# Kernel optimization log

Measured on AMD Instinct MI355X. Metric: run time of the kernel, lower is better.

Reference implementation:

```python
import jax, jax.numpy as jnp
import numpy as np
from jax import lax

B, L, D, H, NW, NL = 4, 256, 768, 384, 4, 9
WINDOWS = (3, 5, 7, 9)


def setup_inputs() -> dict:
    key = jax.random.key(0)
    ks = jax.random.split(key, 12)
    s = 0.05
    return {
        "seq_out": jax.random.normal(ks[0], (B, L, D), jnp.float32),
        "valid_ids": jax.random.randint(ks[1], (B, L), 0, 2),
        "w_ih_f": jax.random.normal(ks[2], (NW, 4 * H, D), jnp.float32) * s,
        "w_hh_f": jax.random.normal(ks[3], (NW, 4 * H, H), jnp.float32) * s,
        "b_ih_f": jax.random.normal(ks[4], (NW, 4 * H), jnp.float32) * s,
        "b_hh_f": jax.random.normal(ks[5], (NW, 4 * H), jnp.float32) * s,
        "w_ih_b": jax.random.normal(ks[6], (NW, 4 * H, D), jnp.float32) * s,
        "w_hh_b": jax.random.normal(ks[7], (NW, 4 * H, H), jnp.float32) * s,
        "b_ih_b": jax.random.normal(ks[8], (NW, 4 * H), jnp.float32) * s,
        "b_hh_b": jax.random.normal(ks[9], (NW, 4 * H), jnp.float32) * s,
        "lin_w": jax.random.normal(ks[10], (NL, D), jnp.float32) * s,
        "lin_b": jnp.zeros((NL,), jnp.float32),
    }


def _lstm_last(win, mask, W_ih, W_hh, b, reverse):
    # invalid (out-of-range) steps leave the state untouched, so the final
    # carry equals the hidden state after the last valid step (PyTorch LSTM math).
    Bx, Lx, w, Dx = win.shape
    Hh = W_hh.shape[1]

    def step(carry, xm):
        h, c = carry
        x_t, m = xm  # [B,L,D], [L]
        gates = x_t @ W_ih.T + h @ W_hh.T + b  # [B,L,4H], gate order i,f,g,o
        i, f, g, o = jnp.split(gates, 4, axis=-1)
        i = jax.nn.sigmoid(i)
        f = jax.nn.sigmoid(f)
        g = jnp.tanh(g)
        o = jax.nn.sigmoid(o)
        c_new = f * c + i * g
        h_new = o * jnp.tanh(c_new)
        m3 = m[None, :, None]
        return (jnp.where(m3, h_new, h), jnp.where(m3, c_new, c)), None

    init = (jnp.zeros((Bx, Lx, Hh), win.dtype), jnp.zeros((Bx, Lx, Hh), win.dtype))
    (h, _), _ = lax.scan(step, init, (jnp.moveaxis(win, 2, 0), mask.T), reverse=reverse)
    return h


def _window_features(x, w, Wif, Whf, bf, Wib, Whb, bb):
    # Faithful vectorization of windows_sequence: the sorted index_list for
    # position i is the contiguous slice [max(0,i-w//2) .. min(L-1,i+w//2)].
    Bx, Lx, Dx = x.shape
    half = w // 2
    pos = jnp.arange(Lx)[:, None] + jnp.arange(-half, half + 1)[None, :]  # [L,w]
    mask = (pos >= 0) & (pos < Lx)
    idx = jnp.clip(pos, 0, Lx - 1)
    win = x[:, idx, :]  # [B,L,w,D]
    h_f = _lstm_last(win, mask, Wif, Whf, bf, reverse=False)  # fwd dir: last output
    h_b = _lstm_last(win, mask, Wib, Whb, bb, reverse=True)   # bwd dir over reversed window
    return jnp.concatenate([h_f, h_b], axis=-1)  # [B,L,D]


def _valid_scatter(x, valid_ids):
    # Left-pack tokens with valid_ids==1 (the nested Python scatter loop).
    Bx, Lx, Dx = x.shape
    v = valid_ids.astype(jnp.int32)
    dest = jnp.where(v == 1, jnp.cumsum(v, axis=1) - 1, Lx)  # invalid -> pad slot

    def pack(row_x, row_d):
        return jnp.zeros((Lx + 1, Dx), row_x.dtype).at[row_d].set(row_x)[:Lx]

    return jax.vmap(pack)(x, dest)


def reference(seq_out, valid_ids, w_ih_f, w_hh_f, b_ih_f, b_hh_f,
              w_ih_b, w_hh_b, b_ih_b, b_hh_b, lin_w, lin_b):
    x = _valid_scatter(seq_out, valid_ids)  # [B,L,D]; dropout is identity in eval
    locals_ = [
        _window_features(x, WINDOWS[i],
                         w_ih_f[i], w_hh_f[i], b_ih_f[i] + b_hh_f[i],
                         w_ih_b[i], w_hh_b[i], b_ih_b[i] + b_hh_b[i])
        for i in range(NW)
    ]
    muti = jnp.stack(locals_, axis=2)  # [B,L,NW,D]
    # dot-att: query is the (packed) sequence output itself
    attn = jax.nn.softmax(
        jnp.einsum('bld,blwd->blw', x, muti) / jnp.sqrt(jnp.float32(D)), axis=-1)
    local_feat = jnp.einsum('blw,blwd->bld', attn, muti)
    out = x + local_feat
    return out @ lin_w.T + lin_b  # logits [B,L,NL]
```

## Files before the change

### kernel.cpp

```cpp
#include <hip/hip_runtime.h>
#include <math.h>

#define LL 256
#define DD 768
#define HH 384
#define G4 1536
#define NWIN 4
#define NLIN 9
#define NPOS 1024
#define PROJ_N 12288
#define HSTRIDE 520

typedef __attribute__((ext_vector_type(8))) short short8;
typedef __attribute__((ext_vector_type(4))) short short4v;
typedef __attribute__((ext_vector_type(16))) float f32x16;

static __device__ __forceinline__ float bf2f(unsigned short u) {
    union { unsigned int i; float f; } v; v.i = ((unsigned int)u) << 16; return v.f;
}
static __device__ __forceinline__ unsigned short f2bf(float f) {
    unsigned int u = __float_as_uint(f);
    u += 0x7fff + ((u >> 16) & 1);
    return (unsigned short)(u >> 16);
}
static __device__ __forceinline__ float fsig(float x) {
    return __builtin_amdgcn_rcpf(1.f + __expf(-x));
}
static __device__ __forceinline__ float ftanh(float x) {
    return 1.f - 2.f * __builtin_amdgcn_rcpf(1.f + __expf(2.f * x));
}

__global__ __launch_bounds__(256) void prep_kernel(
        const float* __restrict__ seq, const int* __restrict__ valid,
        unsigned short* __restrict__ xfrag,
        const float* __restrict__ wihF, const float* __restrict__ wihB,
        unsigned short* __restrict__ wfih,
        const float* __restrict__ whhF, const float* __restrict__ whhB,
        unsigned short* __restrict__ wfhh) {
    const int tid = threadIdx.x;
    if (blockIdx.x < 128) {
        const int b = blockIdx.x >> 5;
        const int chunk = blockIdx.x & 31;
        __shared__ int vbuf[LL];
        __shared__ int dest[LL];
        __shared__ int nvalid;
        vbuf[tid] = valid[b * LL + tid];
        __syncthreads();
        if (tid == 0) {
            int c = 0;
            for (int l = 0; l < LL; ++l) dest[l] = vbuf[l] ? c++ : -1;
            nvalid = c;
        }
        __syncthreads();
        const int nv = nvalid;
        for (int l = chunk * 8; l < chunk * 8 + 8; ++l) {
            const int d = dest[l];
            if (d >= 0) {
                const float* src = seq + (size_t)(b * LL + l) * DD;
                const int pos = b * LL + d;
                const int pt = pos >> 5, pl = pos & 31;
                for (int j = tid; j < DD / 8; j += 256) {
                    const float4 v0 = ((const float4*)src)[2 * j];
                    const float4 v1 = ((const float4*)src)[2 * j + 1];
                    short8 pv;
                    pv[0] = (short)f2bf(v0.x); pv[1] = (short)f2bf(v0.y);
                    pv[2] = (short)f2bf(v0.z); pv[3] = (short)f2bf(v0.w);
                    pv[4] = (short)f2bf(v1.x); pv[5] = (short)f2bf(v1.y);
                    pv[6] = (short)f2bf(v1.z); pv[7] = (short)f2bf(v1.w);
                    *(short8*)(xfrag + ((size_t)(pt * 48 + (j >> 1)) * 512 + (pl + 32 * (j & 1)) * 8)) = pv;
                }
            }
            if (l >= nv) {
                const int pos = b * LL + l;
                const int pt = pos >> 5, pl = pos & 31;
                const short8 zv = {};
                for (int j = tid; j < DD / 8; j += 256)
                    *(short8*)(xfrag + ((size_t)(pt * 48 + (j >> 1)) * 512 + (pl + 32 * (j & 1)) * 8)) = zv;
            }
        }
    } else {
        __shared__ unsigned short lds[32 * 768];
        const int cb = blockIdx.x - 128;
        const int isIH = cb < 384;
        const int vblk = isIH ? cb : (cb - 384);
        const int K = isIH ? DD : HH;
        const float* srcF = isIH ? wihF : whhF;
        const float* srcB = isIH ? wihB : whhB;
        unsigned short* dst = isIH ? wfih : wfhh;
        const int vrow0 = vblk * 32;
        const int chain = vrow0 / G4;
        const int dir = chain >> 2, wi = chain & 3;
        const float* src = (dir ? srcB : srcF) + (size_t)(wi * G4 + (vrow0 % G4)) * K;
        const int total = 32 * K;
        for (int i = tid * 4; i < total; i += 1024) {
            const float4 v = *(const float4*)(src + i);
            lds[i + 0] = f2bf(v.x); lds[i + 1] = f2bf(v.y);
            lds[i + 2] = f2bf(v.z); lds[i + 3] = f2bf(v.w);
        }
        __syncthreads();
        const int nks = K >> 4;
        for (int slot = tid; slot < nks * 64; slot += 256) {
            const int ks = slot >> 6;
            const int lane = slot & 63;
            const int row = lane & 31;
            const int kb = ks * 16 + (lane >> 5) * 8;
            const short8 v = *(const short8*)&lds[row * K + kb];
            *(short8*)(dst + ((size_t)vblk * nks + ks) * 512 + lane * 8) = v;
        }
    }
}

__global__ __launch_bounds__(256) void proj_mfma(
        const unsigned short* __restrict__ xf,
        const unsigned short* __restrict__ wf,
        const float* __restrict__ bihf, const float* __restrict__ bhhf,
        const float* __restrict__ bihb, const float* __restrict__ bhhb,
        unsigned short* __restrict__ proj) {
    __shared__ __align__(16) unsigned short st[4 * 4096];
    const int wv = threadIdx.x >> 6;
    const int lane = threadIdx.x & 63;
    const int colid = lane & 31, hq = lane >> 5;
    const int chain = blockIdx.x & 7;
    const int r8 = blockIdx.x >> 3;
    const int us = r8 % 12;
    const int mtg = r8 / 12;
    const int dir = chain >> 2, wi = chain & 3;

    const unsigned short* bP = wf + (size_t)((chain * 48 + wv * 12 + us) * 48) * 512 + lane * 8;
    const unsigned short* aP = xf + (size_t)(mtg * 4 * 48) * 512 + lane * 8;

    f32x16 acc[4] = {};
#pragma unroll 4
    for (int ks = 0; ks < 48; ++ks) {
        const short8 bv = *(const short8*)(bP + ks * 512);
        const short8 a0 = *(const short8*)(aP + (0 * 48 + ks) * 512);
        const short8 a1 = *(const short8*)(aP + (1 * 48 + ks) * 512);
        const short8 a2 = *(const short8*)(aP + (2 * 48 + ks) * 512);
        const short8 a3 = *(const short8*)(aP + (3 * 48 + ks) * 512);
        acc[0] = __builtin_amdgcn_mfma_f32_32x32x16_bf16(a0, bv, acc[0], 0, 0, 0);
        acc[1] = __builtin_amdgcn_mfma_f32_32x32x16_bf16(a1, bv, acc[1], 0, 0, 0);
        acc[2] = __builtin_amdgcn_mfma_f32_32x32x16_bf16(a2, bv, acc[2], 0, 0, 0);
        acc[3] = __builtin_amdgcn_mfma_f32_32x32x16_bf16(a3, bv, acc[3], 0, 0, 0);
    }
    const int br = wv * HH + us * 32 + colid;
    const float bv = (dir ? bihb : bihf)[wi * G4 + br] + (dir ? bhhb : bhhf)[wi * G4 + br];
#pragma unroll
    for (int i = 0; i < 4; ++i) {
#pragma unroll
        for (int r = 0; r < 16; ++r) {
            const int row = (r & 3) + 8 * (r >> 2) + 4 * hq;
            st[i * 4096 + (row * 32 + colid) * 4 + wv] = f2bf(acc[i][r] + bv);
        }
    }
    __syncthreads();
#pragma unroll
    for (int j = 0; j < 8; ++j) {
        const int idx = j * 256 + threadIdx.x;
        const int i = idx >> 9, rem = idx & 511;
        const int pl = rem >> 4, q = rem & 15;
        const int pos = (mtg * 4 + i) * 32 + pl;
        *(int4*)(proj + (size_t)pos * PROJ_N + chain * G4 + us * 128 + q * 8) =
            ((const int4*)st)[idx];
    }
}

__global__ __launch_bounds__(768, 3) void lstm_fused(
        const unsigned short* __restrict__ Wf,
        const unsigned short* __restrict__ proj,
        unsigned short* __restrict__ hfin) {
    const int p = blockIdx.x & 3, sub = (blockIdx.x >> 2) & 1;
    const int slot = blockIdx.x >> 3;
    const int chainA[4] = {3, 7, 2, 6};
    const int chainB[4] = {0, 4, 1, 5};
    const int chain = (slot < 16) ? chainA[p] : chainB[p];
    const int pt = sub * 16 + (slot & 15);
    const int dir = chain >> 2, wi = chain & 3;
    const int w = 3 + 2 * wi, half = wi + 1;
    const int tid = threadIdx.x;
    const int lane = tid & 63, wv = tid >> 6;
    const int colid = lane & 31, hq = lane >> 5;
    const int uu = wv * 32 + colid;
    const int m0 = pt * 32, b = m0 >> 8, l0 = m0 & 255;

    __shared__ __align__(16) unsigned short Hbuf[2][24 * HSTRIDE];
    float c[16];
#pragma unroll
    for (int r = 0; r < 16; ++r) c[r] = 0.f;

    const unsigned short* projb = proj + (size_t)(b * LL) * PROJ_N + chain * G4 + uu * 4;
    const unsigned short* Wb = Wf + (size_t)((chain * 48 + wv) * 24) * 512 + lane * 8;
    const int ksp = uu >> 4, khp = (uu >> 3) & 1, jp = uu & 7;
    const int hslot = ksp * HSTRIDE + khp * 256 + jp;

    for (int s = 0; s < w; ++s) {
        const int t = dir ? (w - 1 - s) : s;
        const int tmh = t - half;
        unsigned short* cur = Hbuf[s & 1];
        const unsigned short* prev = Hbuf[(s & 1) ^ 1];

        short4v pj[16];
#pragma unroll
        for (int r = 0; r < 16; ++r) {
            const int row = (r & 3) + 8 * (r >> 2) + 4 * hq;
            int src = l0 + row + tmh;
            src = src < 0 ? 0 : (src > LL - 1 ? LL - 1 : src);
            pj[r] = __builtin_nontemporal_load((const short4v*)(projb + src * PROJ_N));
        }

        f32x16 acc0 = {}, acc1 = {}, acc2 = {}, acc3 = {};
        if (s > 0) {
            const unsigned short* Alds = prev + lane * 8;
#pragma unroll 4
            for (int ks = 0; ks < 24; ++ks) {
                const short8 av  = *(const short8*)(Alds + ks * HSTRIDE);
                const short8 bv0 = *(const short8*)(Wb + (size_t)(0 * 288 + ks) * 512);
                const short8 bv1 = *(const short8*)(Wb + (size_t)(1 * 288 + ks) * 512);
                const short8 bv2 = *(const short8*)(Wb + (size_t)(2 * 288 + ks) * 512);
                const short8 bv3 = *(const short8*)(Wb + (size_t)(3 * 288 + ks) * 512);
                acc0 = __builtin_amdgcn_mfma_f32_32x32x16_bf16(av, bv0, acc0, 0, 0, 0);
                acc1 = __builtin_amdgcn_mfma_f32_32x32x16_bf16(av, bv1, acc1, 0, 0, 0);
                acc2 = __builtin_amdgcn_mfma_f32_32x32x16_bf16(av, bv2, acc2, 0, 0, 0);
                acc3 = __builtin_amdgcn_mfma_f32_32x32x16_bf16(av, bv3, acc3, 0, 0, 0);
            }
        }

#pragma unroll
        for (int r = 0; r < 16; ++r) {
            const int row = (r & 3) + 8 * (r >> 2) + 4 * hq;
            const int src = l0 + row + tmh;
            unsigned short hv;
            if (src >= 0 && src < LL) {
                const float gi = acc0[r] + bf2f((unsigned short)pj[r][0]);
                const float gf = acc1[r] + bf2f((unsigned short)pj[r][1]);
                const float gg = acc2[r] + bf2f((unsigned short)pj[r][2]);
                const float go = acc3[r] + bf2f((unsigned short)pj[r][3]);
                c[r] = fsig(gf) * c[r] + fsig(gi) * ftanh(gg);
                hv = f2bf(fsig(go) * ftanh(c[r]));
            } else {
                hv = (s == 0) ? (unsigned short)0 : prev[hslot + row * 8];
            }
            cur[hslot + row * 8] = hv;
        }
        __syncthreads();
    }

    const unsigned short* fin = Hbuf[(w - 1) & 1];
    unsigned short* ho = hfin + (size_t)chain * (NPOS * HH) + (size_t)pt * 12288;
#pragma unroll
    for (int i = tid; i < 1536; i += 768) {
        const int ks = i >> 6, off = i & 63;
        *(int4*)(ho + ks * 512 + off * 8) = *(const int4*)(fin + ks * HSTRIDE + off * 8);
    }
}

__global__ __launch_bounds__(512) void attn_out_kernel(
        const unsigned short* __restrict__ xfrag,
        const unsigned short* __restrict__ hfin,
        const float* __restrict__ lin_w, const float* __restrict__ lin_b,
        float* __restrict__ out) {
    const int pt = blockIdx.x;
    const int tid = threadIdx.x;
    const int lane = tid & 63, wv = tid >> 6;
    const int dir = wv >> 2, kr = wv & 3;
    const int pos = lane & 31, kh = lane >> 5;
    const float inv_sqrt_d = 0.03608439182435161f;

    __shared__ float scp[8][4][32];
    __shared__ float attw[4][32];
    __shared__ float redp[8][32][10];

    const unsigned short* xb = xfrag + ((size_t)(pt * 48 + 24 * dir)) * 512 + lane * 8;
    const unsigned short* hb0 = hfin + (size_t)(dir * 4) * (NPOS * HH) + (size_t)pt * 12288 + lane * 8;

    float sc4[4] = {0.f, 0.f, 0.f, 0.f};
#pragma unroll
    for (int k = 0; k < 6; ++k) {
        const int ks = kr * 6 + k;
        const short8 xv = *(const short8*)(xb + ks * 512);
        float xf[8];
#pragma unroll
        for (int j = 0; j < 8; ++j) xf[j] = bf2f((unsigned short)xv[j]);
#pragma unroll
        for (int wi = 0; wi < 4; ++wi) {
            const short8 hv = *(const short8*)(hb0 + (size_t)wi * (NPOS * HH) + ks * 512);
#pragma unroll
            for (int j = 0; j < 8; ++j)
                sc4[wi] = fmaf(xf[j], bf2f((unsigned short)hv[j]), sc4[wi]);
        }
    }
#pragma unroll
    for (int wi = 0; wi < 4; ++wi) sc4[wi] += __shfl_down(sc4[wi], 32);
    if (lane < 32) {
#pragma unroll
        for (int wi = 0; wi < 4; ++wi) scp[wv][wi][pos] = sc4[wi];
    }
    __syncthreads();
    if (tid < 32) {
        float s[4], mx = -1e30f;
#pragma unroll
        for (int wi = 0; wi < 4; ++wi) {
            float v = 0.f;
#pragma unroll
            for (int g = 0; g < 8; ++g) v += scp[g][wi][tid];
            s[wi] = v * inv_sqrt_d;
            mx = fmaxf(mx, s[wi]);
        }
        float denom = 0.f;
#pragma unroll
        for (int wi = 0; wi < 4; ++wi) { s[wi] = __expf(s[wi] - mx); denom += s[wi]; }
        const float rd = __builtin_amdgcn_rcpf(denom);
#pragma unroll
        for (int wi = 0; wi < 4; ++wi) attw[wi][tid] = s[wi] * rd;
    }
    __syncthreads();

    float aw[4];
#pragma unroll
    for (int wi = 0; wi < 4; ++wi) aw[wi] = attw[wi][pos];
    float rp[9];
#pragma unroll
    for (int r = 0; r < 9; ++r) rp[r] = 0.f;
#pragma unroll
    for (int k = 0; k < 6; ++k) {
        const int ks = kr * 6 + k;
        const short8 xv = *(const short8*)(xb + ks * 512);
        float ov[8];
#pragma unroll
        for (int j = 0; j < 8; ++j) ov[j] = bf2f((unsigned short)xv[j]);
#pragma unroll
        for (int wi = 0; wi < 4; ++wi) {
            const short8 hv = *(const short8*)(hb0 + (size_t)wi * (NPOS * HH) + ks * 512);
#pragma unroll
            for (int j = 0; j < 8; ++j)
                ov[j] = fmaf(aw[wi], bf2f((unsigned short)hv[j]), ov[j]);
        }
        const int dbase = dir * 384 + ks * 16 + kh * 8;
#pragma unroll
        for (int r = 0; r < 9; ++r) {
            const float4 lw0 = *(const float4*)(lin_w + r * DD + dbase);
            const float4 lw1 = *(const float4*)(lin_w + r * DD + dbase + 4);
            rp[r] += ov[0] * lw0.x + ov[1] * lw0.y + ov[2] * lw0.z + ov[3] * lw0.w
                   + ov[4] * lw1.x + ov[5] * lw1.y + ov[6] * lw1.z + ov[7] * lw1.w;
        }
    }
#pragma unroll
    for (int r = 0; r < 9; ++r) rp[r] += __shfl_down(rp[r], 32);
    if (lane < 32) {
#pragma unroll
        for (int r = 0; r < 9; ++r) redp[wv][pos][r] = rp[r];
    }
    __syncthreads();
    if (tid < 288) {
        const int p2 = tid / 9, r = tid % 9;
        float s = lin_b[r];
#pragma unroll
        for (int g = 0; g < 8; ++g) s += redp[g][p2][r];
        out[(size_t)(pt * 32 + p2) * NLIN + r] = s;
    }
}

extern "C" void kernel_launch(void* const* d_in, const int* in_sizes, int n_in,
                              void* d_out, int out_size, void* d_ws, size_t ws_size,
                              hipStream_t stream) {
    (void)in_sizes; (void)n_in; (void)out_size; (void)ws_size;
    const float* seq   = (const float*)d_in[0];
    const int*   valid = (const int*)d_in[1];
    const float* wih_f = (const float*)d_in[2];
    const float* whh_f = (const float*)d_in[3];
    const float* bih_f = (const float*)d_in[4];
    const float* bhh_f = (const float*)d_in[5];
    const float* wih_b = (const float*)d_in[6];
    const float* whh_b = (const float*)d_in[7];
    const float* bih_b = (const float*)d_in[8];
    const float* bhh_b = (const float*)d_in[9];
    const float* lin_w = (const float*)d_in[10];
    const float* lin_b = (const float*)d_in[11];
    float* out = (float*)d_out;

    unsigned short* xfrag = (unsigned short*)d_ws;
    unsigned short* proj  = xfrag + (size_t)NPOS * DD;
    unsigned short* wfhh  = proj + (size_t)NPOS * PROJ_N;
    unsigned short* wfih  = wfhh + (size_t)4718592;
    unsigned short* hfin  = wfih + (size_t)9437184;

    prep_kernel<<<896, 256, 0, stream>>>(seq, valid, xfrag,
                                         wih_f, wih_b, wfih,
                                         whh_f, whh_b, wfhh);
    proj_mfma<<<768, 256, 0, stream>>>(xfrag, wfih, bih_f, bhh_f, bih_b, bhh_b, proj);
    lstm_fused<<<256, 768, 0, stream>>>(wfhh, proj, hfin);
    attn_out_kernel<<<32, 512, 0, stream>>>(xfrag, hfin, lin_w, lin_b, out);
}
```

Before: 290.0 us.

## Process two 32-row M tiles per LSTM block, splitting gate MFMAs into two passes

```diff
diff --git a/kernel.cpp b/kernel.cpp
--- a/kernel.cpp
+++ b/kernel.cpp
@@ -168,24 +168,23 @@
         const unsigned short* __restrict__ Wf,
         const unsigned short* __restrict__ proj,
         unsigned short* __restrict__ hfin) {
-    const int p = blockIdx.x & 3, sub = (blockIdx.x >> 2) & 1;
-    const int slot = blockIdx.x >> 3;
-    const int chainA[4] = {3, 7, 2, 6};
-    const int chainB[4] = {0, 4, 1, 5};
-    const int chain = (slot < 16) ? chainA[p] : chainB[p];
-    const int pt = sub * 16 + (slot & 15);
+    const int x = blockIdx.x & 7;
+    const int s0 = blockIdx.x >> 3;
+    const int pr = x >> 1;
+    int lc = (pr & 1) ? 7 : 3; if (pr & 2) lc -= 1;
+    int sc = ((pr & 1) ? 4 : 0) + ((pr & 2) ? 1 : 0);
+    const int chain = (s0 < 8) ? lc : sc;
+    const int pt64 = (x & 1) * 8 + (s0 & 7);
     const int dir = chain >> 2, wi = chain & 3;
     const int w = 3 + 2 * wi, half = wi + 1;
     const int tid = threadIdx.x;
     const int lane = tid & 63, wv = tid >> 6;
     const int colid = lane & 31, hq = lane >> 5;
     const int uu = wv * 32 + colid;
-    const int m0 = pt * 32, b = m0 >> 8, l0 = m0 & 255;
-
-    __shared__ __align__(16) unsigned short Hbuf[2][24 * HSTRIDE];
-    float c[16];
-#pragma unroll
-    for (int r = 0; r < 16; ++r) c[r] = 0.f;
+    const int m0 = pt64 * 64, b = m0 >> 8, l0 = m0 & 255;
+
+    __shared__ __align__(16) unsigned short Hbuf[2][2 * 24 * HSTRIDE];
+    f32x16 c0 = {}, c1 = {};
 
     const unsigned short* projb = proj + (size_t)(b * LL) * PROJ_N + chain * G4 + uu * 4;
     const unsigned short* Wb = Wf + (size_t)((chain * 48 + wv) * 24) * 512 + lane * 8;
@@ -198,58 +197,140 @@
         unsigned short* cur = Hbuf[s & 1];
         const unsigned short* prev = Hbuf[(s & 1) ^ 1];
 
-        short4v pj[16];
-#pragma unroll
-        for (int r = 0; r < 16; ++r) {
-            const int row = (r & 3) + 8 * (r >> 2) + 4 * hq;
-            int src = l0 + row + tmh;
-            src = src < 0 ? 0 : (src > LL - 1 ? LL - 1 : src);
-            pj[r] = __builtin_nontemporal_load((const short4v*)(projb + src * PROJ_N));
-        }
-
-        f32x16 acc0 = {}, acc1 = {}, acc2 = {}, acc3 = {};
+        f32x16 ai0 = {}, ai1 = {}, af0 = {}, af1 = {};
         if (s > 0) {
-            const unsigned short* Alds = prev + lane * 8;
+            const unsigned short* A0 = prev + lane * 8;
+            const unsigned short* A1 = prev + 24 * HSTRIDE + lane * 8;
 #pragma unroll 4
             for (int ks = 0; ks < 24; ++ks) {
-                const short8 av  = *(const short8*)(Alds + ks * HSTRIDE);
-                const short8 bv0 = *(const short8*)(Wb + (size_t)(0 * 288 + ks) * 512);
-                const short8 bv1 = *(const short8*)(Wb + (size_t)(1 * 288 + ks) * 512);
-                const short8 bv2 = *(const short8*)(Wb + (size_t)(2 * 288 + ks) * 512);
-                const short8 bv3 = *(const short8*)(Wb + (size_t)(3 * 288 + ks) * 512);
-                acc0 = __builtin_amdgcn_mfma_f32_32x32x16_bf16(av, bv0, acc0, 0, 0, 0);
-                acc1 = __builtin_amdgcn_mfma_f32_32x32x16_bf16(av, bv1, acc1, 0, 0, 0);
-                acc2 = __builtin_amdgcn_mfma_f32_32x32x16_bf16(av, bv2, acc2, 0, 0, 0);
-                acc3 = __builtin_amdgcn_mfma_f32_32x32x16_bf16(av, bv3, acc3, 0, 0, 0);
-            }
-        }
-
-#pragma unroll
-        for (int r = 0; r < 16; ++r) {
-            const int row = (r & 3) + 8 * (r >> 2) + 4 * hq;
-            const int src = l0 + row + tmh;
-            unsigned short hv;
-            if (src >= 0 && src < LL) {
-                const float gi = acc0[r] + bf2f((unsigned short)pj[r][0]);
-                const float gf = acc1[r] + bf2f((unsigned short)pj[r][1]);
-                const float gg = acc2[r] + bf2f((unsigned short)pj[r][2]);
-                const float go = acc3[r] + bf2f((unsigned short)pj[r][3]);
-                c[r] = fsig(gf) * c[r] + fsig(gi) * ftanh(gg);
-                hv = f2bf(fsig(go) * ftanh(c[r]));
-            } else {
-                hv = (s == 0) ? (unsigned short)0 : prev[hslot + row * 8];
-            }
-            cur[hslot + row * 8] = hv;
+                const short8 av0 = *(const short8*)(A0 + ks * HSTRIDE);
+                const short8 av1 = *(const short8*)(A1 + ks * HSTRIDE);
+                const short8 bvi = *(const short8*)(Wb + (size_t)(0 * 288 + ks) * 512);
+                const short8 bvf = *(const short8*)(Wb + (size_t)(1 * 288 + ks) * 512);
+                ai0 = __builtin_amdgcn_mfma_f32_32x32x16_bf16(av0, bvi, ai0, 0, 0, 0);
+                ai1 = __builtin_amdgcn_mfma_f32_32x32x16_bf16(av1, bvi, ai1, 0, 0, 0);
+                af0 = __builtin_amdgcn_mfma_f32_32x32x16_bf16(av0, bvf, af0, 0, 0, 0);
+                af1 = __builtin_amdgcn_mfma_f32_32x32x16_bf16(av1, bvf, af1, 0, 0, 0);
+            }
+        }
+        f32x16 si0, si1;
+        {
+            unsigned int pj[16];
+#pragma unroll
+            for (int r = 0; r < 16; ++r) {
+                const int row = (r & 3) + 8 * (r >> 2) + 4 * hq;
+                int src = l0 + row + tmh;
+                src = src < 0 ? 0 : (src > LL - 1 ? LL - 1 : src);
+                pj[r] = __builtin_nontemporal_load((const unsigned int*)(projb + src * PROJ_N));
+            }
+#pragma unroll
+            for (int r = 0; r < 16; ++r) {
+                const int row = (r & 3) + 8 * (r >> 2) + 4 * hq;
+                const int src = l0 + row + tmh;
+                if (src >= 0 && src < LL) {
+                    si0[r] = fsig(ai0[r] + bf2f((unsigned short)(pj[r] & 0xffff)));
+                    c0[r] = c0[r] * fsig(af0[r] + bf2f((unsigned short)(pj[r] >> 16)));
+                }
+            }
+        }
+        {
+            unsigned int pj[16];
+#pragma unroll
+            for (int r = 0; r < 16; ++r) {
+                const int row = (r & 3) + 8 * (r >> 2) + 4 * hq;
+                int src = l0 + 32 + row + tmh;
+                src = src < 0 ? 0 : (src > LL - 1 ? LL - 1 : src);
+                pj[r] = __builtin_nontemporal_load((const unsigned int*)(projb + src * PROJ_N));
+            }
+#pragma unroll
+            for (int r = 0; r < 16; ++r) {
+                const int row = (r & 3) + 8 * (r >> 2) + 4 * hq;
+                const int src = l0 + 32 + row + tmh;
+                if (src >= 0 && src < LL) {
+                    si1[r] = fsig(ai1[r] + bf2f((unsigned short)(pj[r] & 0xffff)));
+                    c1[r] = c1[r] * fsig(af1[r] + bf2f((unsigned short)(pj[r] >> 16)));
+                }
+            }
+        }
+
+        f32x16 ag0 = {}, ag1 = {}, ao0 = {}, ao1 = {};
+        if (s > 0) {
+            const unsigned short* A0 = prev + lane * 8;
+            const unsigned short* A1 = prev + 24 * HSTRIDE + lane * 8;
+#pragma unroll 4
+            for (int ks = 0; ks < 24; ++ks) {
+                const short8 av0 = *(const short8*)(A0 + ks * HSTRIDE);
+                const short8 av1 = *(const short8*)(A1 + ks * HSTRIDE);
+                const short8 bvg = *(const short8*)(Wb + (size_t)(2 * 288 + ks) * 512);
+                const short8 bvo = *(const short8*)(Wb + (size_t)(3 * 288 + ks) * 512);
+                ag0 = __builtin_amdgcn_mfma_f32_32x32x16_bf16(av0, bvg, ag0, 0, 0, 0);
+                ag1 = __builtin_amdgcn_mfma_f32_32x32x16_bf16(av1, bvg, ag1, 0, 0, 0);
+                ao0 = __builtin_amdgcn_mfma_f32_32x32x16_bf16(av0, bvo, ao0, 0, 0, 0);
+                ao1 = __builtin_amdgcn_mfma_f32_32x32x16_bf16(av1, bvo, ao1, 0, 0, 0);
+            }
+        }
+        {
+            unsigned int pj[16];
+#pragma unroll
+            for (int r = 0; r < 16; ++r) {
+                const int row = (r & 3) + 8 * (r >> 2) + 4 * hq;
+                int src = l0 + row + tmh;
+                src = src < 0 ? 0 : (src > LL - 1 ? LL - 1 : src);
+                pj[r] = __builtin_nontemporal_load((const unsigned int*)(projb + src * PROJ_N + 2));
+            }
+#pragma unroll
+            for (int r = 0; r < 16; ++r) {
+                const int row = (r & 3) + 8 * (r >> 2) + 4 * hq;
+                const int src = l0 + row + tmh;
+                unsigned short hv;
+                if (src >= 0 && src < LL) {
+                    const float tg = ftanh(ag0[r] + bf2f((unsigned short)(pj[r] & 0xffff)));
+                    const float so = fsig(ao0[r] + bf2f((unsigned short)(pj[r] >> 16)));
+                    c0[r] = fmaf(si0[r], tg, c0[r]);
+                    hv = f2bf(so * ftanh(c0[r]));
+                } else {
+                    hv = (s == 0) ? (unsigned short)0 : prev[hslot + row * 8];
+                }
+                cur[hslot + row * 8] = hv;
+            }
+        }
+        {
+            unsigned int pj[16];
+#pragma unroll
+            for (int r = 0; r < 16; ++r) {
+                const int row = (r & 3) + 8 * (r >> 2) + 4 * hq;
+                int src = l0 + 32 + row + tmh;
+                src = src < 0 ? 0 : (src > LL - 1 ? LL - 1 : src);
+                pj[r] = __builtin_nontemporal_load((const unsigned int*)(projb + src * PROJ_N + 2));
+            }
+#pragma unroll
+            for (int r = 0; r < 16; ++r) {
+                const int row = (r & 3) + 8 * (r >> 2) + 4 * hq;
+                const int src = l0 + 32 + row + tmh;
+                unsigned short hv;
+                if (src >= 0 && src < LL) {
+                    const float tg = ftanh(ag1[r] + bf2f((unsigned short)(pj[r] & 0xffff)));
+                    const float so = fsig(ao1[r] + bf2f((unsigned short)(pj[r] >> 16)));
+                    c1[r] = fmaf(si1[r], tg, c1[r]);
+                    hv = f2bf(so * ftanh(c1[r]));
+                } else {
+                    hv = (s == 0) ? (unsigned short)0 : prev[24 * HSTRIDE + hslot + row * 8];
+                }
+                cur[24 * HSTRIDE + hslot + row * 8] = hv;
+            }
         }
         __syncthreads();
     }
 
     const unsigned short* fin = Hbuf[(w - 1) & 1];
-    unsigned short* ho = hfin + (size_t)chain * (NPOS * HH) + (size_t)pt * 12288;
-#pragma unroll
-    for (int i = tid; i < 1536; i += 768) {
-        const int ks = i >> 6, off = i & 63;
-        *(int4*)(ho + ks * 512 + off * 8) = *(const int4*)(fin + ks * HSTRIDE + off * 8);
+#pragma unroll
+    for (int mt = 0; mt < 2; ++mt) {
+        unsigned short* ho = hfin + (size_t)chain * (NPOS * HH) + (size_t)(pt64 * 2 + mt) * 12288;
+        const unsigned short* fm = fin + mt * 24 * HSTRIDE;
+        for (int i = tid; i < 1536; i += 768) {
+            const int ks = i >> 6, off = i & 63;
+            *(int4*)(ho + ks * 512 + off * 8) = *(const int4*)(fm + ks * HSTRIDE + off * 8);
+        }
     }
 }
 
@@ -387,6 +468,6 @@
                                          wih_f, wih_b, wfih,
                                          whh_f, whh_b, wfhh);
     proj_mfma<<<768, 256, 0, stream>>>(xfrag, wfih, bih_f, bhh_f, bih_b, bhh_b, proj);
-    lstm_fused<<<256, 768, 0, stream>>>(wfhh, proj, hfin);
+    lstm_fused<<<128, 768, 0, stream>>>(wfhh, proj, hfin);
     attn_out_kernel<<<32, 512, 0, stream>>>(xfrag, hfin, lin_w, lin_b, out);
 }
```

After: 949.3 us. 227% more time.

## Split attention/output into two wider-grid kernels and parallelize valid-token prefix scan

Applied to the files above, without the earlier changes.

```diff
diff --git a/kernel.cpp b/kernel.cpp
--- a/kernel.cpp
+++ b/kernel.cpp
@@ -36,21 +36,26 @@
         const float* __restrict__ wihF, const float* __restrict__ wihB,
         unsigned short* __restrict__ wfih,
         const float* __restrict__ whhF, const float* __restrict__ whhB,
-        unsigned short* __restrict__ wfhh) {
+        unsigned short* __restrict__ wfhh,
+        const float* __restrict__ lin_b, float* __restrict__ out) {
     const int tid = threadIdx.x;
     if (blockIdx.x < 128) {
         const int b = blockIdx.x >> 5;
         const int chunk = blockIdx.x & 31;
-        __shared__ int vbuf[LL];
         __shared__ int dest[LL];
+        __shared__ int wsum[4];
         __shared__ int nvalid;
-        vbuf[tid] = valid[b * LL + tid];
+        const int v = valid[b * LL + tid];
+        const unsigned long long m = __ballot(v != 0);
+        const int lane = tid & 63, wvi = tid >> 6;
+        const int pre = __popcll(m & (((unsigned long long)1 << lane) - 1));
+        if (lane == 63) wsum[wvi] = pre + (v ? 1 : 0);
         __syncthreads();
-        if (tid == 0) {
-            int c = 0;
-            for (int l = 0; l < LL; ++l) dest[l] = vbuf[l] ? c++ : -1;
-            nvalid = c;
-        }
+        int base = 0;
+#pragma unroll
+        for (int k = 0; k < 4; ++k) if (k < wvi) base += wsum[k];
+        dest[tid] = v ? (base + pre) : -1;
+        if (tid == 0) nvalid = wsum[0] + wsum[1] + wsum[2] + wsum[3];
         __syncthreads();
         const int nv = nvalid;
         for (int l = chunk * 8; l < chunk * 8 + 8; ++l) {
@@ -78,7 +83,7 @@
                     *(short8*)(xfrag + ((size_t)(pt * 48 + (j >> 1)) * 512 + (pl + 32 * (j & 1)) * 8)) = zv;
             }
         }
-    } else {
+    } else if (blockIdx.x < 896) {
         __shared__ unsigned short lds[32 * 768];
         const int cb = blockIdx.x - 128;
         const int isIH = cb < 384;
@@ -107,6 +112,9 @@
             const short8 v = *(const short8*)&lds[row * K + kb];
             *(short8*)(dst + ((size_t)vblk * nks + ks) * 512 + lane * 8) = v;
         }
+    } else {
+        for (int i = tid; i < NPOS * NLIN; i += 256)
+            out[i] = lin_b[i % NLIN];
     }
 }
 
@@ -253,76 +261,93 @@
     }
 }
 
-__global__ __launch_bounds__(512) void attn_out_kernel(
+__global__ __launch_bounds__(192) void attn_scores_kernel(
         const unsigned short* __restrict__ xfrag,
         const unsigned short* __restrict__ hfin,
-        const float* __restrict__ lin_w, const float* __restrict__ lin_b,
+        float* __restrict__ scores) {
+    const int pt = blockIdx.x >> 3, seg = blockIdx.x & 7;
+    const int dir = seg >> 2, q = seg & 3;
+    const int tid = threadIdx.x;
+    const int lane = tid & 63, wv3 = tid >> 6;
+    const int pos = lane & 31;
+    __shared__ float scp[3][4][32];
+
+    const unsigned short* xb = xfrag + ((size_t)(pt * 48 + 24 * dir)) * 512 + lane * 8;
+    const unsigned short* hb0 = hfin + (size_t)(dir * 4) * (NPOS * HH) + (size_t)pt * 12288 + lane * 8;
+
+    float sc4[4] = {0.f, 0.f, 0.f, 0.f};
+#pragma unroll
+    for (int k = 0; k < 2; ++k) {
+        const int ks = q * 6 + wv3 * 2 + k;
+        const short8 xv = *(const short8*)(xb + ks * 512);
+        float xf[8];
+#pragma unroll
+        for (int j = 0; j < 8; ++j) xf[j] = bf2f((unsigned short)xv[j]);
+#pragma unroll
+        for (int wi = 0; wi < 4; ++wi) {
+            const short8 hv = *(const short8*)(hb0 + (size_t)wi * (NPOS * HH) + ks * 512);
+#pragma unroll
+            for (int j = 0; j < 8; ++j)
+                sc4[wi] = fmaf(xf[j], bf2f((unsigned short)hv[j]), sc4[wi]);
+        }
+    }
+#pragma unroll
+    for (int wi = 0; wi < 4; ++wi) sc4[wi] += __shfl_down(sc4[wi], 32);
+    if (lane < 32) {
+#pragma unroll
+        for (int wi = 0; wi < 4; ++wi) scp[wv3][wi][pos] = sc4[wi];
+    }
+    __syncthreads();
+    if (tid < 32) {
+#pragma unroll
+        for (int wi = 0; wi < 4; ++wi) {
+            const float v = scp[0][wi][tid] + scp[1][wi][tid] + scp[2][wi][tid];
+            scores[(((size_t)pt * 8 + seg) * 4 + wi) * 32 + tid] = v;
+        }
+    }
+}
+
+__global__ __launch_bounds__(192) void attn_out2_kernel(
+        const unsigned short* __restrict__ xfrag,
+        const unsigned short* __restrict__ hfin,
+        const float* __restrict__ scores,
+        const float* __restrict__ lin_w,
         float* __restrict__ out) {
-    const int pt = blockIdx.x;
+    const int pt = blockIdx.x >> 3, seg = blockIdx.x & 7;
+    const int dir = seg >> 2, q = seg & 3;
     const int tid = threadIdx.x;
-    const int lane = tid & 63, wv = tid >> 6;
-    const int dir = wv >> 2, kr = wv & 3;
+    const int lane = tid & 63, wv3 = tid >> 6;
     const int pos = lane & 31, kh = lane >> 5;
     const float inv_sqrt_d = 0.03608439182435161f;
-
-    __shared__ float scp[8][4][32];
-    __shared__ float attw[4][32];
-    __shared__ float redp[8][32][10];
+    __shared__ float redp[3][32][10];
+
+    float s[4];
+#pragma unroll
+    for (int wi = 0; wi < 4; ++wi) {
+        float v = 0.f;
+#pragma unroll
+        for (int s2 = 0; s2 < 8; ++s2)
+            v += scores[(((size_t)pt * 8 + s2) * 4 + wi) * 32 + pos];
+        s[wi] = v * inv_sqrt_d;
+    }
+    float mx = fmaxf(fmaxf(s[0], s[1]), fmaxf(s[2], s[3]));
+    float denom = 0.f;
+    float aw[4];
+#pragma unroll
+    for (int wi = 0; wi < 4; ++wi) { aw[wi] = __expf(s[wi] - mx); denom += aw[wi]; }
+    const float rd = __builtin_amdgcn_rcpf(denom);
+#pragma unroll
+    for (int wi = 0; wi < 4; ++wi) aw[wi] *= rd;
 
     const unsigned short* xb = xfrag + ((size_t)(pt * 48 + 24 * dir)) * 512 + lane * 8;
     const unsigned short* hb0 = hfin + (size_t)(dir * 4) * (NPOS * HH) + (size_t)pt * 12288 + lane * 8;
 
-    float sc4[4] = {0.f, 0.f, 0.f, 0.f};
-#pragma unroll
-    for (int k = 0; k < 6; ++k) {
-        const int ks = kr * 6 + k;
-        const short8 xv = *(const short8*)(xb + ks * 512);
-        float xf[8];
-#pragma unroll
-        for (int j = 0; j < 8; ++j) xf[j] = bf2f((unsigned short)xv[j]);
-#pragma unroll
-        for (int wi = 0; wi < 4; ++wi) {
-            const short8 hv = *(const short8*)(hb0 + (size_t)wi * (NPOS * HH) + ks * 512);
-#pragma unroll
-            for (int j = 0; j < 8; ++j)
-                sc4[wi] = fmaf(xf[j], bf2f((unsigned short)hv[j]), sc4[wi]);
-        }
-    }
-#pragma unroll
-    for (int wi = 0; wi < 4; ++wi) sc4[wi] += __shfl_down(sc4[wi], 32);
-    if (lane < 32) {
-#pragma unroll
-        for (int wi = 0; wi < 4; ++wi) scp[wv][wi][pos] = sc4[wi];
-    }
-    __syncthreads();
-    if (tid < 32) {
-        float s[4], mx = -1e30f;
-#pragma unroll
-        for (int wi = 0; wi < 4; ++wi) {
-            float v = 0.f;
-#pragma unroll
-            for (int g = 0; g < 8; ++g) v += scp[g][wi][tid];
-            s[wi] = v * inv_sqrt_d;
-            mx = fmaxf(mx, s[wi]);
-        }
-        float denom = 0.f;
-#pragma unroll
-        for (int wi = 0; wi < 4; ++wi) { s[wi] = __expf(s[wi] - mx); denom += s[wi]; }
-        const float rd = __builtin_amdgcn_rcpf(denom);
-#pragma unroll
-        for (int wi = 0; wi < 4; ++wi) attw[wi][tid] = s[wi] * rd;
-    }
-    __syncthreads();
-
-    float aw[4];
-#pragma unroll
-    for (int wi = 0; wi < 4; ++wi) aw[wi] = attw[wi][pos];
     float rp[9];
 #pragma unroll
     for (int r = 0; r < 9; ++r) rp[r] = 0.f;
 #pragma unroll
-    for (int k = 0; k < 6; ++k) {
-        const int ks = kr * 6 + k;
+    for (int k = 0; k < 2; ++k) {
+        const int ks = q * 6 + wv3 * 2 + k;
         const short8 xv = *(const short8*)(xb + ks * 512);
         float ov[8];
 #pragma unroll
@@ -347,15 +372,17 @@
     for (int r = 0; r < 9; ++r) rp[r] += __shfl_down(rp[r], 32);
     if (lane < 32) {
 #pragma unroll
-        for (int r = 0; r < 9; ++r) redp[wv][pos][r] = rp[r];
+        for (int r = 0; r < 9; ++r) redp[wv3][pos][r] = rp[r];
     }
     __syncthreads();
-    if (tid < 288) {
-        const int p2 = tid / 9, r = tid % 9;
-        float s = lin_b[r];
-#pragma unroll
-        for (int g = 0; g < 8; ++g) s += redp[g][p2][r];
-        out[(size_t)(pt * 32 + p2) * NLIN + r] = s;
+    if (tid < 96) {
+#pragma unroll
+        for (int e = 0; e < 3; ++e) {
+            const int flat = tid * 3 + e;
+            const int p2 = flat / 9, r = flat % 9;
+            const float sum = redp[0][p2][r] + redp[1][p2][r] + redp[2][p2][r];
+            atomicAdd(&out[(size_t)(pt * 32 + p2) * NLIN + r], sum);
+        }
     }
 }
 
@@ -382,11 +409,14 @@
     unsigned short* wfhh  = proj + (size_t)NPOS * PROJ_N;
     unsigned short* wfih  = wfhh + (size_t)4718592;
     unsigned short* hfin  = wfih + (size_t)9437184;
-
-    prep_kernel<<<896, 256, 0, stream>>>(seq, valid, xfrag,
+    float* scores = (float*)(hfin + (size_t)3145728);
+
+    prep_kernel<<<897, 256, 0, stream>>>(seq, valid, xfrag,
                                          wih_f, wih_b, wfih,
-                                         whh_f, whh_b, wfhh);
+                                         whh_f, whh_b, wfhh,
+                                         lin_b, out);
     proj_mfma<<<768, 256, 0, stream>>>(xfrag, wfih, bih_f, bhh_f, bih_b, bhh_b, proj);
     lstm_fused<<<256, 768, 0, stream>>>(wfhh, proj, hfin);
-    attn_out_kernel<<<32, 512, 0, stream>>>(xfrag, hfin, lin_w, lin_b, out);
-}
+    attn_scores_kernel<<<256, 192, 0, stream>>>(xfrag, hfin, scores);
+    attn_out2_kernel<<<256, 192, 0, stream>>>(xfrag, hfin, scores, lin_w, out);
+}
```

New measurement: 283.3 us. 2.3% less time.
